# Kernel optimization log

Hardware: AMD Instinct MI355X
Metric: run time of the kernel (lower is better)

Reference implementation:

```python
import jax, jax.numpy as jnp
import numpy as np

EPS = 1e-12  # torch F.normalize default eps


def _l2norm(x):
    return x / jnp.maximum(jnp.linalg.norm(x, axis=-1, keepdims=True), EPS)


def setup_inputs() -> dict:
    key = jax.random.key(0)
    k1, k2, k3, k4 = jax.random.split(key, 4)
    B, N, F = 2048, 128, 256
    drug = jax.random.normal(k1, (B, N, F), dtype=jnp.float32)
    cell = jax.random.normal(k2, (B, F), dtype=jnp.float32)
    # xavier_uniform bound for square [F,F]: sqrt(6/(F+F))
    bound = float(np.sqrt(6.0 / (F + F)))
    k = jax.random.uniform(k3, (F, F), minval=-bound, maxval=bound, dtype=jnp.float32)
    q = jax.random.uniform(k4, (F, F), minval=-bound, maxval=bound, dtype=jnp.float32)
    return {"drug": drug, "cell": cell, "k": k, "q": q}


def reference(drug, cell, k, q):
    d = _l2norm(drug)                 # [B, N, F]
    c = _l2norm(cell[:, None, :])     # [B, 1, F]
    drug_ = d @ k                     # [B, N, F]
    cell_ = c @ q                     # [B, 1, F]
    scores = jnp.einsum('bof,bnf->bon', cell_, drug_)  # [B, 1, N]
    attn = jax.nn.softmax(scores, axis=2)
    sim = jnp.einsum('bof,bnf->bon', c, d)             # [B, 1, N]
    return (attn * sim)[:, 0, :]      # [B, N]
```

## Files before the change

### kernel.cpp

```cpp
#include <hip/hip_runtime.h>
#include <math.h>

#define F 256
#define NROW 128
#define EPS 1e-12f

__global__ __launch_bounds__(256) void l2norm_rows(const float* __restrict__ x,
                                                   float* __restrict__ out,
                                                   int nrows) {
    int wave = blockIdx.x * 4 + (threadIdx.x >> 6);
    int lane = threadIdx.x & 63;
    if (wave >= nrows) return;
    const float4* xr = (const float4*)(x + (size_t)wave * F);
    float4 v = xr[lane];
    float s = v.x * v.x + v.y * v.y + v.z * v.z + v.w * v.w;
#pragma unroll
    for (int m = 1; m < 64; m <<= 1) s += __shfl_xor(s, m, 64);
    float inv = 1.0f / fmaxf(sqrtf(s), EPS);
    float4 o = {v.x * inv, v.y * inv, v.z * inv, v.w * inv};
    ((float4*)(out + (size_t)wave * F))[lane] = o;
}

__global__ __launch_bounds__(256) void qkT_kernel(const float* __restrict__ q,
                                                  const float* __restrict__ k,
                                                  float* __restrict__ M) {
    __shared__ float qs[F];
    int f = blockIdx.x;
    qs[threadIdx.x] = q[(size_t)f * F + threadIdx.x];
    __syncthreads();
    int g = threadIdx.x;
    const float4* kr = (const float4*)(k + (size_t)g * F);
    const float4* qr = (const float4*)qs;
    float acc = 0.f;
#pragma unroll 8
    for (int j = 0; j < F / 4; j++) {
        float4 kv = kr[j];
        float4 qv = qr[j];
        acc += kv.x * qv.x + kv.y * qv.y + kv.z * qv.z + kv.w * qv.w;
    }
    M[(size_t)f * F + g] = acc;
}

__global__ __launch_bounds__(256) void w_gemm(const float* __restrict__ CN,
                                              const float* __restrict__ M,
                                              float* __restrict__ W) {
    __shared__ float As[32][64];
    __shared__ float Bs[64][64];
    int rb = blockIdx.x * 32;
    int cb = blockIdx.y * 64;
    int tid = threadIdx.x;
    int colq = tid & 15;
    int rowp = tid >> 4;
    float acc[2][4] = {{0.f, 0.f, 0.f, 0.f}, {0.f, 0.f, 0.f, 0.f}};
    for (int k0 = 0; k0 < F; k0 += 64) {
        __syncthreads();
#pragma unroll
        for (int e = 0; e < 2; e++) {
            int s = tid + e * 256;
            int r = s >> 4;
            int c = (s & 15) << 2;
            *(float4*)&As[r][c] = *(const float4*)&CN[(size_t)(rb + r) * F + k0 + c];
        }
#pragma unroll
        for (int e = 0; e < 4; e++) {
            int s = tid + e * 256;
            int r = s >> 4;
            int c = (s & 15) << 2;
            *(float4*)&Bs[r][c] = *(const float4*)&M[(size_t)(k0 + r) * F + cb + c];
        }
        __syncthreads();
#pragma unroll
        for (int kk = 0; kk < 64; kk++) {
            float4 b4 = *(const float4*)&Bs[kk][colq * 4];
            float a0 = As[rowp * 2 + 0][kk];
            float a1 = As[rowp * 2 + 1][kk];
            acc[0][0] += a0 * b4.x; acc[0][1] += a0 * b4.y;
            acc[0][2] += a0 * b4.z; acc[0][3] += a0 * b4.w;
            acc[1][0] += a1 * b4.x; acc[1][1] += a1 * b4.y;
            acc[1][2] += a1 * b4.z; acc[1][3] += a1 * b4.w;
        }
    }
#pragma unroll
    for (int r = 0; r < 2; r++) {
        float4 o = {acc[r][0], acc[r][1], acc[r][2], acc[r][3]};
        *(float4*)&W[(size_t)(rb + rowp * 2 + r) * F + cb + colq * 4] = o;
    }
}

__global__ __launch_bounds__(256) void fused_main(const float* __restrict__ drug,
                                                  const float* __restrict__ CN,
                                                  const float* __restrict__ W,
                                                  float* __restrict__ out) {
    int b = blockIdx.x;
    int tid = threadIdx.x;
    int wave = tid >> 6;
    int lane = tid & 63;
    int grp = lane >> 4;
    int l16 = lane & 15;

    __shared__ float sc[NROW];
    __shared__ float sm[NROW];
    __shared__ float red[4];

    const float* wrow = W + (size_t)b * F;
    const float* crow = CN + (size_t)b * F;
    float4 w4[4], c4[4];
#pragma unroll
    for (int j = 0; j < 4; j++) {
        w4[j] = *(const float4*)&wrow[j * 64 + l16 * 4];
        c4[j] = *(const float4*)&crow[j * 64 + l16 * 4];
    }

    const float* dbase = drug + (size_t)b * NROW * F;
#pragma unroll 2
    for (int it = 0; it < 8; it++) {
        int n = wave * 32 + it * 4 + grp;
        const float* drow = dbase + (size_t)n * F;
        float an = 0.f, aw = 0.f, ac = 0.f;
#pragma unroll
        for (int j = 0; j < 4; j++) {
            float4 v = *(const float4*)&drow[j * 64 + l16 * 4];
            an += v.x * v.x + v.y * v.y + v.z * v.z + v.w * v.w;
            aw += v.x * w4[j].x + v.y * w4[j].y + v.z * w4[j].z + v.w * w4[j].w;
            ac += v.x * c4[j].x + v.y * c4[j].y + v.z * c4[j].z + v.w * c4[j].w;
        }
#pragma unroll
        for (int m = 1; m < 16; m <<= 1) {
            an += __shfl_xor(an, m, 64);
            aw += __shfl_xor(aw, m, 64);
            ac += __shfl_xor(ac, m, 64);
        }
        if (l16 == 0) {
            float inv = 1.0f / fmaxf(sqrtf(an), EPS);
            sc[n] = aw * inv;
            sm[n] = ac * inv;
        }
    }
    __syncthreads();

    float s = sc[tid & 127];
    float v = s;
#pragma unroll
    for (int m = 1; m < 64; m <<= 1) v = fmaxf(v, __shfl_xor(v, m, 64));
    if (lane == 0) red[wave] = v;
    __syncthreads();
    float gmax = fmaxf(fmaxf(red[0], red[1]), fmaxf(red[2], red[3]));
    float e = expf(s - gmax);
    float t = (tid < NROW) ? e : 0.f;
#pragma unroll
    for (int m = 1; m < 64; m <<= 1) t += __shfl_xor(t, m, 64);
    __syncthreads();
    if (lane == 0) red[wave] = t;
    __syncthreads();
    float tot = red[0] + red[1] + red[2] + red[3];
    if (tid < NROW) {
        out[(size_t)b * NROW + tid] = (e / tot) * sm[tid & 127];
    }
}

extern "C" void kernel_launch(void* const* d_in, const int* in_sizes, int n_in,
                              void* d_out, int out_size, void* d_ws, size_t ws_size,
                              hipStream_t stream) {
    const float* drug = (const float*)d_in[0];
    const float* cell = (const float*)d_in[1];
    const float* k = (const float*)d_in[2];
    const float* q = (const float*)d_in[3];
    float* out = (float*)d_out;

    int B = in_sizes[1] / F;

    float* CN = (float*)d_ws;
    float* M = CN + (size_t)B * F;
    float* W = M + (size_t)F * F;

    l2norm_rows<<<dim3((B + 3) / 4), dim3(256), 0, stream>>>(cell, CN, B);
    qkT_kernel<<<dim3(F), dim3(256), 0, stream>>>(q, k, M);
    w_gemm<<<dim3(B / 32, F / 64), dim3(256), 0, stream>>>(CN, M, W);
    fused_main<<<dim3(B), dim3(256), 0, stream>>>(drug, CN, W, out);
}
```

Before: 384.1 us.

## Fold cell normalization into main kernel, drop l2norm launch, nontemporal drug loads

Removes the separate cell l2norm kernel: the raw cell is fed to the W GEMM, and the main kernel computes the cell norm itself and folds its inverse into the per-row scale. The W GEMM inner loop is restructured so each wave handles 8 rows with scalar B loads. Drug loads switch to nontemporal loads to avoid polluting cache with streamed data. This saves one launch and a workspace round trip, at the cost of a slightly different GEMM register/LDS access pattern.

New measurement: 363.6 us. -5.3%, faster.

```diff
diff --git a/kernel.cpp b/kernel.cpp
--- a/kernel.cpp
+++ b/kernel.cpp
@@ -5,21 +5,7 @@
 #define NROW 128
 #define EPS 1e-12f
 
-__global__ __launch_bounds__(256) void l2norm_rows(const float* __restrict__ x,
-                                                   float* __restrict__ out,
-                                                   int nrows) {
-    int wave = blockIdx.x * 4 + (threadIdx.x >> 6);
-    int lane = threadIdx.x & 63;
-    if (wave >= nrows) return;
-    const float4* xr = (const float4*)(x + (size_t)wave * F);
-    float4 v = xr[lane];
-    float s = v.x * v.x + v.y * v.y + v.z * v.z + v.w * v.w;
-#pragma unroll
-    for (int m = 1; m < 64; m <<= 1) s += __shfl_xor(s, m, 64);
-    float inv = 1.0f / fmaxf(sqrtf(s), EPS);
-    float4 o = {v.x * inv, v.y * inv, v.z * inv, v.w * inv};
-    ((float4*)(out + (size_t)wave * F))[lane] = o;
-}
+typedef float vf4 __attribute__((ext_vector_type(4)));
 
 __global__ __launch_bounds__(256) void qkT_kernel(const float* __restrict__ q,
                                                   const float* __restrict__ k,
@@ -41,7 +27,7 @@
     M[(size_t)f * F + g] = acc;
 }
 
-__global__ __launch_bounds__(256) void w_gemm(const float* __restrict__ CN,
+__global__ __launch_bounds__(256) void w_gemm(const float* __restrict__ cell,
                                               const float* __restrict__ M,
                                               float* __restrict__ W) {
     __shared__ float As[32][64];
@@ -49,9 +35,9 @@
     int rb = blockIdx.x * 32;
     int cb = blockIdx.y * 64;
     int tid = threadIdx.x;
-    int colq = tid & 15;
-    int rowp = tid >> 4;
-    float acc[2][4] = {{0.f, 0.f, 0.f, 0.f}, {0.f, 0.f, 0.f, 0.f}};
+    int wave = tid >> 6;
+    int lane = tid & 63;
+    float acc[8] = {0.f, 0.f, 0.f, 0.f, 0.f, 0.f, 0.f, 0.f};
     for (int k0 = 0; k0 < F; k0 += 64) {
         __syncthreads();
 #pragma unroll
@@ -59,7 +45,7 @@
             int s = tid + e * 256;
             int r = s >> 4;
             int c = (s & 15) << 2;
-            *(float4*)&As[r][c] = *(const float4*)&CN[(size_t)(rb + r) * F + k0 + c];
+            *(float4*)&As[r][c] = *(const float4*)&cell[(size_t)(rb + r) * F + k0 + c];
         }
 #pragma unroll
         for (int e = 0; e < 4; e++) {
@@ -69,27 +55,24 @@
             *(float4*)&Bs[r][c] = *(const float4*)&M[(size_t)(k0 + r) * F + cb + c];
         }
         __syncthreads();
+#pragma unroll 4
+        for (int kk = 0; kk < 64; kk++) {
+            float bv = Bs[kk][lane];
 #pragma unroll
-        for (int kk = 0; kk < 64; kk++) {
-            float4 b4 = *(const float4*)&Bs[kk][colq * 4];
-            float a0 = As[rowp * 2 + 0][kk];
-            float a1 = As[rowp * 2 + 1][kk];
-            acc[0][0] += a0 * b4.x; acc[0][1] += a0 * b4.y;
-            acc[0][2] += a0 * b4.z; acc[0][3] += a0 * b4.w;
-            acc[1][0] += a1 * b4.x; acc[1][1] += a1 * b4.y;
-            acc[1][2] += a1 * b4.z; acc[1][3] += a1 * b4.w;
+            for (int r = 0; r < 8; r++) {
+                acc[r] += As[wave * 8 + r][kk] * bv;
+            }
         }
     }
 #pragma unroll
-    for (int r = 0; r < 2; r++) {
-        float4 o = {acc[r][0], acc[r][1], acc[r][2], acc[r][3]};
-        *(float4*)&W[(size_t)(rb + rowp * 2 + r) * F + cb + colq * 4] = o;
+    for (int r = 0; r < 8; r++) {
+        W[(size_t)(rb + wave * 8 + r) * F + cb + lane] = acc[r];
     }
 }
 
 __global__ __launch_bounds__(256) void fused_main(const float* __restrict__ drug,
-                                                  const float* __restrict__ CN,
-                                                  const float* __restrict__ W,
+                                                  const float* __restrict__ cell,
+                                                  const float* __restrict__ Wraw,
                                                   float* __restrict__ out) {
     int b = blockIdx.x;
     int tid = threadIdx.x;
@@ -102,14 +85,19 @@
     __shared__ float sm[NROW];
     __shared__ float red[4];
 
-    const float* wrow = W + (size_t)b * F;
-    const float* crow = CN + (size_t)b * F;
-    float4 w4[4], c4[4];
+    const float* wrow = Wraw + (size_t)b * F;
+    const float* crow = cell + (size_t)b * F;
+    vf4 w4[4], c4[4];
+    float cs = 0.f;
 #pragma unroll
     for (int j = 0; j < 4; j++) {
-        w4[j] = *(const float4*)&wrow[j * 64 + l16 * 4];
-        c4[j] = *(const float4*)&crow[j * 64 + l16 * 4];
+        w4[j] = *(const vf4*)&wrow[j * 64 + l16 * 4];
+        c4[j] = *(const vf4*)&crow[j * 64 + l16 * 4];
+        cs += c4[j].x * c4[j].x + c4[j].y * c4[j].y + c4[j].z * c4[j].z + c4[j].w * c4[j].w;
     }
+#pragma unroll
+    for (int m = 1; m < 16; m <<= 1) cs += __shfl_xor(cs, m, 64);
+    float invc = 1.0f / fmaxf(sqrtf(cs), EPS);
 
     const float* dbase = drug + (size_t)b * NROW * F;
 #pragma unroll 2
@@ -119,7 +107,7 @@
         float an = 0.f, aw = 0.f, ac = 0.f;
 #pragma unroll
         for (int j = 0; j < 4; j++) {
-            float4 v = *(const float4*)&drow[j * 64 + l16 * 4];
+            vf4 v = __builtin_nontemporal_load((const vf4*)&drow[j * 64 + l16 * 4]);
             an += v.x * v.x + v.y * v.y + v.z * v.z + v.w * v.w;
             aw += v.x * w4[j].x + v.y * w4[j].y + v.z * w4[j].z + v.w * w4[j].w;
             ac += v.x * c4[j].x + v.y * c4[j].y + v.z * c4[j].z + v.w * c4[j].w;
@@ -131,7 +119,7 @@
             ac += __shfl_xor(ac, m, 64);
         }
         if (l16 == 0) {
-            float inv = 1.0f / fmaxf(sqrtf(an), EPS);
+            float inv = invc / fmaxf(sqrtf(an), EPS);
             sc[n] = aw * inv;
             sm[n] = ac * inv;
         }
@@ -169,12 +157,10 @@
 
     int B = in_sizes[1] / F;
 
-    float* CN = (float*)d_ws;
-    float* M = CN + (size_t)B * F;
+    float* M = (float*)d_ws;
     float* W = M + (size_t)F * F;
 
-    l2norm_rows<<<dim3((B + 3) / 4), dim3(256), 0, stream>>>(cell, CN, B);
     qkT_kernel<<<dim3(F), dim3(256), 0, stream>>>(q, k, M);
-    w_gemm<<<dim3(B / 32, F / 64), dim3(256), 0, stream>>>(CN, M, W);
-    fused_main<<<dim3(B), dim3(256), 0, stream>>>(drug, CN, W, out);
+    w_gemm<<<dim3(B / 32, F / 64), dim3(256), 0, stream>>>(cell, M, W);
+    fused_main<<<dim3(B), dim3(256), 0, stream>>>(drug, cell, W, out);
 }
```
